# Performance work log

Hardware: AMD Instinct MI355X
Metric: run time of the kernel (lower is better)

The kernel has to match this reference:

```python
import jax, jax.numpy as jnp
import numpy as np


def setup_inputs() -> dict:
    key = jax.random.key(0)
    k1, k2, k3, k4 = jax.random.split(key, 4)
    B, C, H, W = 4, 48, 512, 512
    T, ws = 3, 64
    # factor matrices (per TensorMultiplication_einsum, T summation terms)
    # init scale: 1/(init_temperature**(1/3) * sqrt(out_dim)) with init_temperature=1.0
    Ws = jax.random.normal(k2, (T, ws, ws), jnp.float32) / np.sqrt(ws)
    Hs = jax.random.normal(k3, (T, ws, ws), jnp.float32) / np.sqrt(ws)
    Cs = jax.random.normal(k4, (T, C, C), jnp.float32) / np.sqrt(C)
    x = jax.random.normal(k1, (B, C, H, W), jnp.float32)
    return {"x": x, "Ws": Ws, "Hs": Hs, "Cs": Cs, "window_size": ws}


def reference(x, Ws, Hs, Cs, window_size):
    """FeatureProcessingBlock forward:
      window_partition -> sum_t einsum('bchw,wW,hH,cC->bCHW') -> window_reverse.
    The window partition/reverse reshapes are fused into one einsum over the
    blocked view (p,q index the window grid; h,w index within-window pixels).
    """
    B, C, H, W = x.shape
    ws = window_size
    # (B, C, H//ws, ws, W//ws, ws)
    xb = x.reshape(B, C, H // ws, ws, W // ws, ws)
    # sum over T terms and contract w, h, c axes with their factor matrices
    out = jnp.einsum('bcphqw,twW,thH,tcC->bCpHqW', xb, Ws, Hs, Cs)
    return out.reshape(B, C, H, W)
```

## Files before the change

### kernel.cpp

```cpp
#include <hip/hip_runtime.h>
#include <hip/hip_bf16.h>


typedef __attribute__((ext_vector_type(8))) short short8;
typedef __attribute__((ext_vector_type(4))) short short4v;
typedef __attribute__((ext_vector_type(4))) float float4v;

#define SMEM_BYTES 120336

static __device__ __forceinline__ unsigned short f2bf(float f) {
  return __builtin_bit_cast(unsigned short, __float2bfloat16(f));
}
static __device__ __forceinline__ unsigned long long pk4(float a, float b, float c, float d) {
  unsigned long long lo = (unsigned int)((unsigned int)f2bf(a) | ((unsigned int)f2bf(b) << 16));
  unsigned long long hi = (unsigned int)((unsigned int)f2bf(c) | ((unsigned int)f2bf(d) << 16));
  return lo | (hi << 32);
}

__global__ __launch_bounds__(512, 2)
void fpb5(const float* __restrict__ x, const float* __restrict__ Ws,
          const float* __restrict__ Hsm, const float* __restrict__ Cs,
          float* __restrict__ out) {
  extern __shared__ char smem[];
  char* Y1F = smem;
  char* Zb  = smem + 49152;
  char* Cf  = smem + 106496;
  char* z16 = smem + 120320;

  int wid = (blockIdx.x & 7) * 128 + (blockIdx.x >> 3);
  int window = wid >> 2, tile = wid & 3;
  int b = window >> 6, p = (window >> 3) & 7, q = window & 7;
  int j0 = tile * 16;

  int tid = threadIdx.x, lane = tid & 63, wave = tid >> 6;
  int lq = lane >> 4, lc = lane & 15;
  int mt = wave & 3, cp = wave >> 2;

  if (tid < 4) ((unsigned int*)z16)[tid] = 0;

  for (int idx = wave; idx < 18; idx += 8) {
    int ss = idx / 3, m = idx - 3 * ss;
    if (lq < 3) {
      short8 v;
      #pragma unroll
      for (int e = 0; e < 8; ++e)
        v[e] = (short)f2bf(Cs[lq * 2304 + (8 * ss + e) * 48 + 16 * m + lc]);
      *(short8*)(Cf + (idx * 16 + lc) * 48 + lq * 16) = v;
    }
  }

  short8 wsf[3][2], hsf[3][2];
  #pragma unroll
  for (int t = 0; t < 3; ++t)
    #pragma unroll
    for (int sv = 0; sv < 2; ++sv) {
      short8 aa, bb;
      #pragma unroll
      for (int e = 0; e < 8; ++e) {
        int k = 32 * sv + 8 * lq + e;
        aa[e] = (short)f2bf(Ws [t * 4096 + k * 64 + j0 + lc]);
        bb[e] = (short)f2bf(Hsm[t * 4096 + k * 64 + 16 * mt + lc]);
      }
      wsf[t][sv] = aa; hsf[t][sv] = bb;
    }

  float4v acc[3][8];
  #pragma unroll
  for (int m = 0; m < 3; ++m)
    #pragma unroll
    for (int i = 0; i < 8; ++i) acc[m][i] = float4v{0.f, 0.f, 0.f, 0.f};

  const float* xbase = x + (((size_t)b * 48) * 512 + p * 64) * 512 + q * 64
                         + (size_t)wave * 262144 + (size_t)lc * 512 + 8 * lq;

  float4v fin[2][8];
  #pragma unroll
  for (int h = 0; h < 2; ++h) {
    const float* src = xbase + (size_t)(32 * h) * 512;
    #pragma unroll
    for (int j2 = 0; j2 < 2; ++j2) {
      const float* r = src + (size_t)(16 * j2) * 512;
      fin[h][4*j2+0] = *(const float4v*)(r);
      fin[h][4*j2+1] = *(const float4v*)(r + 4);
      fin[h][4*j2+2] = *(const float4v*)(r + 32);
      fin[h][4*j2+3] = *(const float4v*)(r + 36);
    }
  }

  for (int s = 0; s < 6; ++s) {
    #pragma unroll
    for (int h = 0; h < 2; ++h) {
      short8 af[4];
      #pragma unroll
      for (int j2 = 0; j2 < 2; ++j2) {
        short8 a0, a1;
        #pragma unroll
        for (int e2 = 0; e2 < 4; ++e2) {
          a0[e2]   = (short)f2bf(fin[h][4*j2+0][e2]);
          a0[4+e2] = (short)f2bf(fin[h][4*j2+1][e2]);
          a1[e2]   = (short)f2bf(fin[h][4*j2+2][e2]);
          a1[4+e2] = (short)f2bf(fin[h][4*j2+3][e2]);
        }
        af[2*j2] = a0; af[2*j2+1] = a1;
      }
      if (s < 5) {
        const float* src = xbase + (size_t)(s + 1) * 2097152 + (size_t)(32 * h) * 512;
        #pragma unroll
        for (int j2 = 0; j2 < 2; ++j2) {
          const float* r = src + (size_t)(16 * j2) * 512;
          fin[h][4*j2+0] = *(const float4v*)(r);
          fin[h][4*j2+1] = *(const float4v*)(r + 4);
          fin[h][4*j2+2] = *(const float4v*)(r + 32);
          fin[h][4*j2+3] = *(const float4v*)(r + 36);
        }
      }
      #pragma unroll
      for (int j2 = 0; j2 < 2; ++j2) {
        int mA = 2 * h + j2;
        int sv  = mA >> 1;
        int lqp = (2 * mA + (lq >> 1)) & 3;
        int eo  = (lq & 1) * 8;
        #pragma unroll
        for (int t = 0; t < 3; ++t) {
          float4v d = {0.f, 0.f, 0.f, 0.f};
          d = __builtin_amdgcn_mfma_f32_16x16x32_bf16(af[2*j2],   wsf[t][0], d, 0, 0, 0);
          d = __builtin_amdgcn_mfma_f32_16x16x32_bf16(af[2*j2+1], wsf[t][1], d, 0, 0, 0);
          short4v pv;
          pv[0] = (short)f2bf(d[0]); pv[1] = (short)f2bf(d[1]);
          pv[2] = (short)f2bf(d[2]); pv[3] = (short)f2bf(d[3]);
          *(short4v*)(Y1F + ((t * 8 + wave) * 2 + sv) * 1024
                          + (lqp * 16 + lc) * 16 + eo) = pv;
        }
      }
    }
    __syncthreads();

    #pragma unroll
    for (int t = 0; t < 3; ++t) {
      float4v dB[4];
      #pragma unroll
      for (int cj = 0; cj < 4; ++cj) {
        const char* yb = Y1F + ((t * 8 + 4 * cp + cj) * 2) * 1024 + lane * 16;
        short8 y0 = *(const short8*)yb;
        short8 y1 = *(const short8*)(yb + 1024);
        float4v dd = {0.f, 0.f, 0.f, 0.f};
        dd = __builtin_amdgcn_mfma_f32_16x16x32_bf16(hsf[t][0], y0, dd, 0, 0, 0);
        dd = __builtin_amdgcn_mfma_f32_16x16x32_bf16(hsf[t][1], y1, dd, 0, 0, 0);
        dB[cj] = dd;
      }
      #pragma unroll
      for (int r = 0; r < 4; ++r) {
        int px = (16 * mt + 4 * lq + r) * 16 + lc;
        *(unsigned long long*)(Zb + px * 56 + 16 * t + 8 * cp) =
            pk4(dB[0][r], dB[1][r], dB[2][r], dB[3][r]);
      }
    }
    __syncthreads();

    {
      short8 cf[3];
      #pragma unroll
      for (int m = 0; m < 3; ++m) {
        const char* csrc = (lq < 3) ? (Cf + ((s * 3 + m) * 16 + lc) * 48 + lq * 16) : z16;
        cf[m] = *(const short8*)csrc;
      }
      #pragma unroll
      for (int i = 0; i < 8; ++i) {
        int px = 16 * (wave + 8 * i) + lc;
        const char* zsrc = (lq < 3) ? (Zb + px * 56 + 16 * lq) : z16;
        short8 zf = *(const short8*)zsrc;
        acc[0][i] = __builtin_amdgcn_mfma_f32_16x16x32_bf16(cf[0], zf, acc[0][i], 0, 0, 0);
        acc[1][i] = __builtin_amdgcn_mfma_f32_16x16x32_bf16(cf[1], zf, acc[1][i], 0, 0, 0);
        acc[2][i] = __builtin_amdgcn_mfma_f32_16x16x32_bf16(cf[2], zf, acc[2][i], 0, 0, 0);
      }
    }
  }

  #pragma unroll
  for (int m = 0; m < 3; ++m)
    #pragma unroll
    for (int i = 0; i < 8; ++i) {
      int n = wave + 8 * i;
      size_t rowbase = (((size_t)(b * 48 + 16 * m + 4 * lq)) * 512 + p * 64 + n) * 512
                       + q * 64 + j0 + lc;
      #pragma unroll
      for (int r = 0; r < 4; ++r)
        out[rowbase + (size_t)r * 262144] = acc[m][i][r];
    }
}

extern "C" void kernel_launch(void* const* d_in, const int* in_sizes, int n_in,
                              void* d_out, int out_size, void* d_ws, size_t ws_size,
                              hipStream_t stream) {
  (void)in_sizes; (void)n_in; (void)d_ws; (void)ws_size; (void)out_size;
  const float* x   = (const float*)d_in[0];
  const float* Ws  = (const float*)d_in[1];
  const float* Hsm = (const float*)d_in[2];
  const float* Cs  = (const float*)d_in[3];
  float* out = (float*)d_out;
  (void)hipFuncSetAttribute((const void*)fpb5,
                            hipFuncAttributeMaxDynamicSharedMemorySize, SMEM_BYTES);
  fpb5<<<dim3(1024), dim3(512), SMEM_BYTES, stream>>>(x, Ws, Hsm, Cs, out);
}
```

Baseline: 183.8 us.

## Make H-contraction wave-local and swizzle padded LDS layouts for Z and C

Each wave now runs the H-factor contraction on its own channel slice, reading its own Y1 tile back from LDS, so Y1 results no longer cross waves. H factor fragments move from registers into a shared LDS table. Z and C buffers switch to a 64-byte padded, XOR-swizzled layout with a zero fourth term, which removes the conditional zero-buffer reads and aims to cut bank conflicts. In exchange there is more LDS traffic for the H fragments, a larger LDS footprint, and a barrier at the end of every iteration to protect Zb reuse.

```diff
diff --git a/kernel.cpp b/kernel.cpp
--- a/kernel.cpp
+++ b/kernel.cpp
@@ -6,7 +6,7 @@
 typedef __attribute__((ext_vector_type(4))) short short4v;
 typedef __attribute__((ext_vector_type(4))) float float4v;
 
-#define SMEM_BYTES 120336
+#define SMEM_BYTES 157696
 
 static __device__ __forceinline__ unsigned short f2bf(float f) {
   return __builtin_bit_cast(unsigned short, __float2bfloat16(f));
@@ -18,14 +18,14 @@
 }
 
 __global__ __launch_bounds__(512, 2)
-void fpb5(const float* __restrict__ x, const float* __restrict__ Ws,
+void fpb6(const float* __restrict__ x, const float* __restrict__ Ws,
           const float* __restrict__ Hsm, const float* __restrict__ Cs,
           float* __restrict__ out) {
   extern __shared__ char smem[];
   char* Y1F = smem;
   char* Zb  = smem + 49152;
-  char* Cf  = smem + 106496;
-  char* z16 = smem + 120320;
+  char* Hf  = smem + 114688;
+  char* Cf  = smem + 139264;
 
   int wid = (blockIdx.x & 7) * 128 + (blockIdx.x >> 3);
   int window = wid >> 2, tile = wid & 3;
@@ -34,34 +34,41 @@
 
   int tid = threadIdx.x, lane = tid & 63, wave = tid >> 6;
   int lq = lane >> 4, lc = lane & 15;
-  int mt = wave & 3, cp = wave >> 2;
-
-  if (tid < 4) ((unsigned int*)z16)[tid] = 0;
-
-  for (int idx = wave; idx < 18; idx += 8) {
-    int ss = idx / 3, m = idx - 3 * ss;
-    if (lq < 3) {
-      short8 v;
-      #pragma unroll
-      for (int e = 0; e < 8; ++e)
-        v[e] = (short)f2bf(Cs[lq * 2304 + (8 * ss + e) * 48 + 16 * m + lc]);
-      *(short8*)(Cf + (idx * 16 + lc) * 48 + lq * 16) = v;
-    }
-  }
-
-  short8 wsf[3][2], hsf[3][2];
+
+  for (int j = wave; j < 24; j += 8) {
+    int mt = j / 6, r6 = j - 6 * mt, t = r6 >> 1, sv = r6 & 1;
+    short8 v;
+    #pragma unroll
+    for (int e = 0; e < 8; ++e) {
+      int h = 32 * sv + 8 * lq + e;
+      v[e] = (short)f2bf(Hsm[t * 4096 + h * 64 + 16 * mt + lc]);
+    }
+    *(short8*)(Hf + (j * 64 + lane) * 16) = v;
+  }
+  for (int row = wave; row < 18; row += 8) {
+    int ss = row / 3, m = row - 3 * ss;
+    short8 v;
+    #pragma unroll
+    for (int e = 0; e < 8; ++e) {
+      int k = 8 * lq + e, c = k >> 2, t = k & 3;
+      v[e] = (t < 3) ? (short)f2bf(Cs[t * 2304 + (8 * ss + c) * 48 + 16 * m + lc])
+                     : (short)0;
+    }
+    *(short8*)(Cf + ((((row * 16 + lc) * 64) + 16 * lq) ^ ((lc & 3) << 4))) = v;
+  }
+
+  short8 wsf[3][2];
   #pragma unroll
   for (int t = 0; t < 3; ++t)
     #pragma unroll
     for (int sv = 0; sv < 2; ++sv) {
-      short8 aa, bb;
+      short8 aa;
       #pragma unroll
       for (int e = 0; e < 8; ++e) {
         int k = 32 * sv + 8 * lq + e;
-        aa[e] = (short)f2bf(Ws [t * 4096 + k * 64 + j0 + lc]);
-        bb[e] = (short)f2bf(Hsm[t * 4096 + k * 64 + 16 * mt + lc]);
-      }
-      wsf[t][sv] = aa; hsf[t][sv] = bb;
+        aa[e] = (short)f2bf(Ws[t * 4096 + k * 64 + j0 + lc]);
+      }
+      wsf[t][sv] = aa;
     }
 
   float4v acc[3][8];
@@ -87,6 +94,10 @@
     }
   }
 
+  __syncthreads();
+
+  char* y1w = Y1F + wave * 6144;
+
   for (int s = 0; s < 6; ++s) {
     #pragma unroll
     for (int h = 0; h < 2; ++h) {
@@ -116,7 +127,7 @@
       }
       #pragma unroll
       for (int j2 = 0; j2 < 2; ++j2) {
-        int mA = 2 * h + j2;
+        int mA  = 2 * h + j2;
         int sv  = mA >> 1;
         int lqp = (2 * mA + (lq >> 1)) & 3;
         int eo  = (lq & 1) * 8;
@@ -128,31 +139,36 @@
           short4v pv;
           pv[0] = (short)f2bf(d[0]); pv[1] = (short)f2bf(d[1]);
           pv[2] = (short)f2bf(d[2]); pv[3] = (short)f2bf(d[3]);
-          *(short4v*)(Y1F + ((t * 8 + wave) * 2 + sv) * 1024
-                          + (lqp * 16 + lc) * 16 + eo) = pv;
-        }
-      }
-    }
-    __syncthreads();
-
-    #pragma unroll
-    for (int t = 0; t < 3; ++t) {
-      float4v dB[4];
-      #pragma unroll
-      for (int cj = 0; cj < 4; ++cj) {
-        const char* yb = Y1F + ((t * 8 + 4 * cp + cj) * 2) * 1024 + lane * 16;
-        short8 y0 = *(const short8*)yb;
-        short8 y1 = *(const short8*)(yb + 1024);
-        float4v dd = {0.f, 0.f, 0.f, 0.f};
-        dd = __builtin_amdgcn_mfma_f32_16x16x32_bf16(hsf[t][0], y0, dd, 0, 0, 0);
-        dd = __builtin_amdgcn_mfma_f32_16x16x32_bf16(hsf[t][1], y1, dd, 0, 0, 0);
-        dB[cj] = dd;
-      }
-      #pragma unroll
-      for (int r = 0; r < 4; ++r) {
-        int px = (16 * mt + 4 * lq + r) * 16 + lc;
-        *(unsigned long long*)(Zb + px * 56 + 16 * t + 8 * cp) =
-            pk4(dB[0][r], dB[1][r], dB[2][r], dB[3][r]);
+          *(short4v*)(y1w + (t * 2 + sv) * 1024 + (lqp * 16 + lc) * 16 + eo) = pv;
+        }
+      }
+    }
+
+    {
+      short8 y0[3], y1[3];
+      #pragma unroll
+      for (int t = 0; t < 3; ++t) {
+        y0[t] = *(const short8*)(y1w + (t * 2 + 0) * 1024 + lane * 16);
+        y1[t] = *(const short8*)(y1w + (t * 2 + 1) * 1024 + lane * 16);
+      }
+      #pragma unroll
+      for (int mt = 0; mt < 4; ++mt) {
+        float4v dB[3];
+        #pragma unroll
+        for (int t = 0; t < 3; ++t) {
+          short8 hf0 = *(const short8*)(Hf + ((mt * 6 + t * 2 + 0) * 64 + lane) * 16);
+          short8 hf1 = *(const short8*)(Hf + ((mt * 6 + t * 2 + 1) * 64 + lane) * 16);
+          float4v dd = {0.f, 0.f, 0.f, 0.f};
+          dd = __builtin_amdgcn_mfma_f32_16x16x32_bf16(hf0, y0[t], dd, 0, 0, 0);
+          dd = __builtin_amdgcn_mfma_f32_16x16x32_bf16(hf1, y1[t], dd, 0, 0, 0);
+          dB[t] = dd;
+        }
+        #pragma unroll
+        for (int r = 0; r < 4; ++r) {
+          int px = (16 * mt + 4 * lq + r) * 16 + lc;
+          *(unsigned long long*)(Zb + ((px * 64 + 8 * wave) ^ ((px & 3) << 4))) =
+              pk4(dB[0][r], dB[1][r], dB[2][r], 0.f);
+        }
       }
     }
     __syncthreads();
@@ -160,20 +176,19 @@
     {
       short8 cf[3];
       #pragma unroll
-      for (int m = 0; m < 3; ++m) {
-        const char* csrc = (lq < 3) ? (Cf + ((s * 3 + m) * 16 + lc) * 48 + lq * 16) : z16;
-        cf[m] = *(const short8*)csrc;
-      }
+      for (int m = 0; m < 3; ++m)
+        cf[m] = *(const short8*)(Cf + (((((s * 3 + m) * 16 + lc) * 64) + 16 * lq)
+                                       ^ ((lc & 3) << 4)));
       #pragma unroll
       for (int i = 0; i < 8; ++i) {
         int px = 16 * (wave + 8 * i) + lc;
-        const char* zsrc = (lq < 3) ? (Zb + px * 56 + 16 * lq) : z16;
-        short8 zf = *(const short8*)zsrc;
+        short8 zf = *(const short8*)(Zb + ((px * 64 + 16 * lq) ^ ((px & 3) << 4)));
         acc[0][i] = __builtin_amdgcn_mfma_f32_16x16x32_bf16(cf[0], zf, acc[0][i], 0, 0, 0);
         acc[1][i] = __builtin_amdgcn_mfma_f32_16x16x32_bf16(cf[1], zf, acc[1][i], 0, 0, 0);
         acc[2][i] = __builtin_amdgcn_mfma_f32_16x16x32_bf16(cf[2], zf, acc[2][i], 0, 0, 0);
       }
     }
+    __syncthreads();
   }
 
   #pragma unroll
@@ -198,7 +213,7 @@
   const float* Hsm = (const float*)d_in[2];
   const float* Cs  = (const float*)d_in[3];
   float* out = (float*)d_out;
-  (void)hipFuncSetAttribute((const void*)fpb5,
+  (void)hipFuncSetAttribute((const void*)fpb6,
                             hipFuncAttributeMaxDynamicSharedMemorySize, SMEM_BYTES);
-  fpb5<<<dim3(1024), dim3(512), SMEM_BYTES, stream>>>(x, Ws, Hsm, Cs, out);
-}
+  fpb6<<<dim3(1024), dim3(512), SMEM_BYTES, stream>>>(x, Ws, Hsm, Cs, out);
+}
```

After: 204.3 us. 11.1% more time.

## Restructure kernel to 1024-thread blocks with merged H and C stages

Applied to the files above, without the earlier changes.

Doubles threads per block from 512 to 1024 and halves the per-wave work in every stage. Ws and Hs factors move from registers into shared memory, Cs is read from global each step instead of from a staged LDS copy, and the H-stage and C-stage now share one barrier, leaving two per step instead of three. The Zb layout changes to a channel-quartered layout that drops the zero-padding fallback, and the next-step x prefetch is moved after the barrier. The aim is more latency hiding and fewer syncs per step. In exchange, occupancy is limited to one large block per CU and shared-memory traffic for the factor reads goes up.

```diff
diff --git a/kernel.cpp b/kernel.cpp
--- a/kernel.cpp
+++ b/kernel.cpp
@@ -6,26 +6,21 @@
 typedef __attribute__((ext_vector_type(4))) short short4v;
 typedef __attribute__((ext_vector_type(4))) float float4v;
 
-#define SMEM_BYTES 120336
+#define SMEM_BYTES 145408
 
 static __device__ __forceinline__ unsigned short f2bf(float f) {
   return __builtin_bit_cast(unsigned short, __float2bfloat16(f));
 }
-static __device__ __forceinline__ unsigned long long pk4(float a, float b, float c, float d) {
-  unsigned long long lo = (unsigned int)((unsigned int)f2bf(a) | ((unsigned int)f2bf(b) << 16));
-  unsigned long long hi = (unsigned int)((unsigned int)f2bf(c) | ((unsigned int)f2bf(d) << 16));
-  return lo | (hi << 32);
-}
-
-__global__ __launch_bounds__(512, 2)
-void fpb5(const float* __restrict__ x, const float* __restrict__ Ws,
+
+__global__ __launch_bounds__(1024)
+void fpb7(const float* __restrict__ x, const float* __restrict__ Ws,
           const float* __restrict__ Hsm, const float* __restrict__ Cs,
           float* __restrict__ out) {
   extern __shared__ char smem[];
   char* Y1F = smem;
   char* Zb  = smem + 49152;
-  char* Cf  = smem + 106496;
-  char* z16 = smem + 120320;
+  char* Hf  = smem + 114688;
+  char* Wf  = smem + 139264;
 
   int wid = (blockIdx.x & 7) * 128 + (blockIdx.x >> 3);
   int window = wid >> 2, tile = wid & 3;
@@ -34,141 +29,148 @@
 
   int tid = threadIdx.x, lane = tid & 63, wave = tid >> 6;
   int lq = lane >> 4, lc = lane & 15;
-  int mt = wave & 3, cp = wave >> 2;
-
-  if (tid < 4) ((unsigned int*)z16)[tid] = 0;
-
-  for (int idx = wave; idx < 18; idx += 8) {
-    int ss = idx / 3, m = idx - 3 * ss;
-    if (lq < 3) {
-      short8 v;
-      #pragma unroll
-      for (int e = 0; e < 8; ++e)
-        v[e] = (short)f2bf(Cs[lq * 2304 + (8 * ss + e) * 48 + 16 * m + lc]);
-      *(short8*)(Cf + (idx * 16 + lc) * 48 + lq * 16) = v;
-    }
-  }
-
-  short8 wsf[3][2], hsf[3][2];
-  #pragma unroll
-  for (int t = 0; t < 3; ++t)
-    #pragma unroll
-    for (int sv = 0; sv < 2; ++sv) {
-      short8 aa, bb;
-      #pragma unroll
-      for (int e = 0; e < 8; ++e) {
-        int k = 32 * sv + 8 * lq + e;
-        aa[e] = (short)f2bf(Ws [t * 4096 + k * 64 + j0 + lc]);
-        bb[e] = (short)f2bf(Hsm[t * 4096 + k * 64 + 16 * mt + lc]);
-      }
-      wsf[t][sv] = aa; hsf[t][sv] = bb;
-    }
-
-  float4v acc[3][8];
+
+  int cA  = wave & 7, hh = wave >> 3;
+  int mtB = wave & 3, cq = wave >> 2;
+
+  if (wave < 6) {
+    int t = wave >> 1, sv = wave & 1;
+    short8 v;
+    #pragma unroll
+    for (int e = 0; e < 8; ++e)
+      v[e] = (short)f2bf(Ws[t * 4096 + (32 * sv + 8 * lq + e) * 64 + j0 + lc]);
+    *(short8*)(Wf + wave * 1024 + lane * 16) = v;
+  }
+  for (int j = wave; j < 24; j += 16) {
+    int mt = j / 6, r6 = j - 6 * mt, t = r6 >> 1, sv = r6 & 1;
+    short8 v;
+    #pragma unroll
+    for (int e = 0; e < 8; ++e)
+      v[e] = (short)f2bf(Hsm[t * 4096 + (32 * sv + 8 * lq + e) * 64 + 16 * mt + lc]);
+    *(short8*)(Hf + j * 1024 + lane * 16) = v;
+  }
+
+  float4v acc[3][4];
   #pragma unroll
   for (int m = 0; m < 3; ++m)
     #pragma unroll
-    for (int i = 0; i < 8; ++i) acc[m][i] = float4v{0.f, 0.f, 0.f, 0.f};
-
-  const float* xbase = x + (((size_t)b * 48) * 512 + p * 64) * 512 + q * 64
-                         + (size_t)wave * 262144 + (size_t)lc * 512 + 8 * lq;
-
-  float4v fin[2][8];
+    for (int i = 0; i < 4; ++i) acc[m][i] = float4v{0.f, 0.f, 0.f, 0.f};
+
+  const float* sA = x + (((size_t)b * 48) * 512 + p * 64) * 512 + q * 64
+                      + (size_t)cA * 262144 + (size_t)lc * 512 + 8 * lq;
+
+  float4v fin[8];
   #pragma unroll
-  for (int h = 0; h < 2; ++h) {
-    const float* src = xbase + (size_t)(32 * h) * 512;
-    #pragma unroll
-    for (int j2 = 0; j2 < 2; ++j2) {
-      const float* r = src + (size_t)(16 * j2) * 512;
-      fin[h][4*j2+0] = *(const float4v*)(r);
-      fin[h][4*j2+1] = *(const float4v*)(r + 4);
-      fin[h][4*j2+2] = *(const float4v*)(r + 32);
-      fin[h][4*j2+3] = *(const float4v*)(r + 36);
-    }
-  }
+  for (int j2 = 0; j2 < 2; ++j2) {
+    const float* r = sA + (size_t)(2 * hh + j2) * 8192;
+    fin[4*j2+0] = *(const float4v*)(r);
+    fin[4*j2+1] = *(const float4v*)(r + 4);
+    fin[4*j2+2] = *(const float4v*)(r + 32);
+    fin[4*j2+3] = *(const float4v*)(r + 36);
+  }
+
+  __syncthreads();
 
   for (int s = 0; s < 6; ++s) {
-    #pragma unroll
-    for (int h = 0; h < 2; ++h) {
+    {
       short8 af[4];
       #pragma unroll
       for (int j2 = 0; j2 < 2; ++j2) {
         short8 a0, a1;
         #pragma unroll
         for (int e2 = 0; e2 < 4; ++e2) {
-          a0[e2]   = (short)f2bf(fin[h][4*j2+0][e2]);
-          a0[4+e2] = (short)f2bf(fin[h][4*j2+1][e2]);
-          a1[e2]   = (short)f2bf(fin[h][4*j2+2][e2]);
-          a1[4+e2] = (short)f2bf(fin[h][4*j2+3][e2]);
+          a0[e2]   = (short)f2bf(fin[4*j2+0][e2]);
+          a0[4+e2] = (short)f2bf(fin[4*j2+1][e2]);
+          a1[e2]   = (short)f2bf(fin[4*j2+2][e2]);
+          a1[4+e2] = (short)f2bf(fin[4*j2+3][e2]);
         }
         af[2*j2] = a0; af[2*j2+1] = a1;
       }
-      if (s < 5) {
-        const float* src = xbase + (size_t)(s + 1) * 2097152 + (size_t)(32 * h) * 512;
+      #pragma unroll
+      for (int t = 0; t < 3; ++t) {
+        short8 wf0 = *(const short8*)(Wf + (t * 2 + 0) * 1024 + lane * 16);
+        short8 wf1 = *(const short8*)(Wf + (t * 2 + 1) * 1024 + lane * 16);
         #pragma unroll
         for (int j2 = 0; j2 < 2; ++j2) {
-          const float* r = src + (size_t)(16 * j2) * 512;
-          fin[h][4*j2+0] = *(const float4v*)(r);
-          fin[h][4*j2+1] = *(const float4v*)(r + 4);
-          fin[h][4*j2+2] = *(const float4v*)(r + 32);
-          fin[h][4*j2+3] = *(const float4v*)(r + 36);
-        }
-      }
-      #pragma unroll
-      for (int j2 = 0; j2 < 2; ++j2) {
-        int mA = 2 * h + j2;
-        int sv  = mA >> 1;
-        int lqp = (2 * mA + (lq >> 1)) & 3;
-        int eo  = (lq & 1) * 8;
-        #pragma unroll
-        for (int t = 0; t < 3; ++t) {
           float4v d = {0.f, 0.f, 0.f, 0.f};
-          d = __builtin_amdgcn_mfma_f32_16x16x32_bf16(af[2*j2],   wsf[t][0], d, 0, 0, 0);
-          d = __builtin_amdgcn_mfma_f32_16x16x32_bf16(af[2*j2+1], wsf[t][1], d, 0, 0, 0);
+          d = __builtin_amdgcn_mfma_f32_16x16x32_bf16(af[2*j2],   wf0, d, 0, 0, 0);
+          d = __builtin_amdgcn_mfma_f32_16x16x32_bf16(af[2*j2+1], wf1, d, 0, 0, 0);
+          int lqp = (2 * j2 + (lq >> 1)) & 3;
           short4v pv;
           pv[0] = (short)f2bf(d[0]); pv[1] = (short)f2bf(d[1]);
           pv[2] = (short)f2bf(d[2]); pv[3] = (short)f2bf(d[3]);
-          *(short4v*)(Y1F + ((t * 8 + wave) * 2 + sv) * 1024
-                          + (lqp * 16 + lc) * 16 + eo) = pv;
+          *(short4v*)(Y1F + ((t * 8 + cA) * 2 + hh) * 1024
+                          + (lqp * 16 + lc) * 16 + (lq & 1) * 8) = pv;
         }
       }
     }
     __syncthreads();
 
-    #pragma unroll
-    for (int t = 0; t < 3; ++t) {
-      float4v dB[4];
-      #pragma unroll
-      for (int cj = 0; cj < 4; ++cj) {
-        const char* yb = Y1F + ((t * 8 + 4 * cp + cj) * 2) * 1024 + lane * 16;
-        short8 y0 = *(const short8*)yb;
-        short8 y1 = *(const short8*)(yb + 1024);
-        float4v dd = {0.f, 0.f, 0.f, 0.f};
-        dd = __builtin_amdgcn_mfma_f32_16x16x32_bf16(hsf[t][0], y0, dd, 0, 0, 0);
-        dd = __builtin_amdgcn_mfma_f32_16x16x32_bf16(hsf[t][1], y1, dd, 0, 0, 0);
-        dB[cj] = dd;
-      }
-      #pragma unroll
-      for (int r = 0; r < 4; ++r) {
-        int px = (16 * mt + 4 * lq + r) * 16 + lc;
-        *(unsigned long long*)(Zb + px * 56 + 16 * t + 8 * cp) =
-            pk4(dB[0][r], dB[1][r], dB[2][r], dB[3][r]);
-      }
-    }
-    __syncthreads();
-
     {
+      float craw[3][6];
+      #pragma unroll
+      for (int m = 0; m < 3; ++m)
+        #pragma unroll
+        for (int ch = 0; ch < 2; ++ch)
+          #pragma unroll
+          for (int t = 0; t < 3; ++t)
+            craw[m][ch*3+t] =
+                Cs[t * 2304 + (8 * s + 2 * lq + ch) * 48 + 16 * m + lc];
+
+      unsigned long long w64[2][4];
+      #pragma unroll
+      for (int t = 0; t < 3; ++t) {
+        short8 hf0 = *(const short8*)(Hf + (mtB * 6 + t * 2 + 0) * 1024 + lane * 16);
+        short8 hf1 = *(const short8*)(Hf + (mtB * 6 + t * 2 + 1) * 1024 + lane * 16);
+        #pragma unroll
+        for (int cj = 0; cj < 2; ++cj) {
+          const char* yb = Y1F + ((t * 8 + 2 * cq + cj) * 2) * 1024 + lane * 16;
+          short8 y0 = *(const short8*)yb;
+          short8 y1 = *(const short8*)(yb + 1024);
+          float4v dd = {0.f, 0.f, 0.f, 0.f};
+          dd = __builtin_amdgcn_mfma_f32_16x16x32_bf16(hf0, y0, dd, 0, 0, 0);
+          dd = __builtin_amdgcn_mfma_f32_16x16x32_bf16(hf1, y1, dd, 0, 0, 0);
+          #pragma unroll
+          for (int r = 0; r < 4; ++r) {
+            unsigned long long v = (unsigned long long)f2bf(dd[r]) << (16 * t);
+            if (t == 0) w64[cj][r] = v; else w64[cj][r] |= v;
+          }
+        }
+      }
+      #pragma unroll
+      for (int cj = 0; cj < 2; ++cj)
+        #pragma unroll
+        for (int r = 0; r < 4; ++r) {
+          int px = (16 * mtB + 4 * lq + r) * 16 + lc;
+          *(unsigned long long*)(Zb + cq * 16384 + px * 16 + cj * 8) = w64[cj][r];
+        }
+
       short8 cf[3];
       #pragma unroll
       for (int m = 0; m < 3; ++m) {
-        const char* csrc = (lq < 3) ? (Cf + ((s * 3 + m) * 16 + lc) * 48 + lq * 16) : z16;
-        cf[m] = *(const short8*)csrc;
-      }
-      #pragma unroll
-      for (int i = 0; i < 8; ++i) {
-        int px = 16 * (wave + 8 * i) + lc;
-        const char* zsrc = (lq < 3) ? (Zb + px * 56 + 16 * lq) : z16;
-        short8 zf = *(const short8*)zsrc;
+        short8 v;
+        v[0] = (short)f2bf(craw[m][0]); v[1] = (short)f2bf(craw[m][1]);
+        v[2] = (short)f2bf(craw[m][2]); v[3] = 0;
+        v[4] = (short)f2bf(craw[m][3]); v[5] = (short)f2bf(craw[m][4]);
+        v[6] = (short)f2bf(craw[m][5]); v[7] = 0;
+        cf[m] = v;
+      }
+      __syncthreads();
+
+      if (s < 5) {
+        #pragma unroll
+        for (int j2 = 0; j2 < 2; ++j2) {
+          const float* r = sA + (size_t)(s + 1) * 2097152 + (size_t)(2 * hh + j2) * 8192;
+          fin[4*j2+0] = *(const float4v*)(r);
+          fin[4*j2+1] = *(const float4v*)(r + 4);
+          fin[4*j2+2] = *(const float4v*)(r + 32);
+          fin[4*j2+3] = *(const float4v*)(r + 36);
+        }
+      }
+      #pragma unroll
+      for (int i = 0; i < 4; ++i) {
+        int px = (wave + 16 * i) * 16 + lc;
+        short8 zf = *(const short8*)(Zb + lq * 16384 + px * 16);
         acc[0][i] = __builtin_amdgcn_mfma_f32_16x16x32_bf16(cf[0], zf, acc[0][i], 0, 0, 0);
         acc[1][i] = __builtin_amdgcn_mfma_f32_16x16x32_bf16(cf[1], zf, acc[1][i], 0, 0, 0);
         acc[2][i] = __builtin_amdgcn_mfma_f32_16x16x32_bf16(cf[2], zf, acc[2][i], 0, 0, 0);
@@ -179,13 +181,12 @@
   #pragma unroll
   for (int m = 0; m < 3; ++m)
     #pragma unroll
-    for (int i = 0; i < 8; ++i) {
-      int n = wave + 8 * i;
-      size_t rowbase = (((size_t)(b * 48 + 16 * m + 4 * lq)) * 512 + p * 64 + n) * 512
-                       + q * 64 + j0 + lc;
+    for (int i = 0; i < 4; ++i) {
+      int n = wave + 16 * i;
       #pragma unroll
       for (int r = 0; r < 4; ++r)
-        out[rowbase + (size_t)r * 262144] = acc[m][i][r];
+        out[(((size_t)(b * 48 + 16 * m + 4 * lq + r)) * 512 + p * 64 + n) * 512
+            + q * 64 + j0 + lc] = acc[m][i][r];
     }
 }
 
@@ -198,7 +199,7 @@
   const float* Hsm = (const float*)d_in[2];
   const float* Cs  = (const float*)d_in[3];
   float* out = (float*)d_out;
-  (void)hipFuncSetAttribute((const void*)fpb5,
+  (void)hipFuncSetAttribute((const void*)fpb7,
                             hipFuncAttributeMaxDynamicSharedMemorySize, SMEM_BYTES);
-  fpb5<<<dim3(1024), dim3(512), SMEM_BYTES, stream>>>(x, Ws, Hsm, Cs, out);
+  fpb7<<<dim3(1024), dim3(1024), SMEM_BYTES, stream>>>(x, Ws, Hsm, Cs, out);
 }
```

Result: faster. 177.3 us (-3.5%).
